# Optimization experiments

Hardware: AMD Instinct MI355X
Metric: run time of the kernel (lower is better)

## Reference

```python
import jax, jax.numpy as jnp
import numpy as np

B, S, H = 32, 4096, 768   # tuples, seq len, longformer hidden
N = 2048                  # total signals across all tuples (segments)
T = 16384                 # total pooled token indices (flattened ragged lists)
C = 32                    # char_size side features
D1, D2 = 512, 512         # MLP hidden dims


def setup_inputs() -> dict:
    key = jax.random.key(0)
    ks = jax.random.split(key, 9)
    hidden_states = jax.random.normal(ks[0], (B, S, H), dtype=jnp.float32)
    base_characteristics = jax.random.normal(ks[1], (N, C), dtype=jnp.float32)
    # MLP params: Linear(768+C,512) -> ReLU -> Linear(512,512) -> ReLU -> Linear(512,1) -> Sigmoid
    w1 = jax.random.normal(ks[2], (H + C, D1), dtype=jnp.float32) * 0.02
    b1 = jnp.zeros((D1,), dtype=jnp.float32)
    w2 = jax.random.normal(ks[3], (D1, D2), dtype=jnp.float32) * 0.02
    b2 = jnp.zeros((D2,), dtype=jnp.float32)
    w3 = jax.random.normal(ks[4], (D2, 1), dtype=jnp.float32) * 0.02
    b3 = jnp.zeros((1,), dtype=jnp.float32)
    # Flattened ragged pooling indices: token_indices index into flattened [B*S] tokens,
    # segment_ids map each index to its (tuple, signal) segment in [0, N).
    token_indices = jax.random.randint(ks[5], (T,), 0, B * S, dtype=jnp.int64)
    segment_ids = jnp.sort(jax.random.randint(ks[6], (T,), 0, N, dtype=jnp.int64))
    return {
        "hidden_states": hidden_states,
        "base_characteristics": base_characteristics,
        "w1": w1, "b1": b1, "w2": w2, "b2": b2, "w3": w3, "b3": b3,
        "token_indices": token_indices,
        "segment_ids": segment_ids,
    }


def reference(hidden_states, base_characteristics, w1, b1, w2, b2, w3, b3,
              token_indices, segment_ids):
    # Gather pooled token embeddings and segment-mean per signal.
    flat = hidden_states.reshape(-1, H)                       # [B*S, H]
    gathered = flat[token_indices]                            # [T, H]
    sums = jax.ops.segment_sum(gathered, segment_ids, num_segments=N)  # [N, H]
    counts = jax.ops.segment_sum(jnp.ones((T,), flat.dtype), segment_ids,
                                 num_segments=N)              # [N]
    pooled = sums / jnp.maximum(counts, 1.0)[:, None]         # mean pool per signal
    feats = jnp.concatenate([pooled, base_characteristics], axis=1)  # [N, H+C]
    h = jax.nn.relu(feats @ w1 + b1)
    h = jax.nn.relu(h @ w2 + b2)
    score = jax.nn.sigmoid(h @ w3 + b3)                       # [N, 1]
    return score.T                                            # [1, N], matches .T in torch
```

## Files before the change

kernel.cpp:

```cpp
#include <hip/hip_runtime.h>
#include <hip/hip_bf16.h>
#include <math.h>

#define BATCH 32
#define SEQ   4096
#define HID   768
#define CHR   32
#define NSEG  2048
#define TTOK  16384
#define KF    (HID + CHR)
#define D1    512
#define D2    512

__global__ __launch_bounds__(256) void pool_kernel(
    const float* __restrict__ hs,
    const float* __restrict__ basec,
    const int*   __restrict__ tok,
    const int*   __restrict__ seg,
    float*       __restrict__ feats)
{
    const int n   = blockIdx.x;
    const int tid = threadIdx.x;

    int lo;
    {
        int l = 0, r = TTOK;
        while (l < r) { int m = (l + r) >> 1; if (seg[m] < n) l = m + 1; else r = m; }
        lo = l;
    }
    int hi;
    {
        int l = lo, r = TTOK;
        while (l < r) { int m = (l + r) >> 1; if (seg[m] < n + 1) l = m + 1; else r = m; }
        hi = l;
    }

    float a0 = 0.f, a1 = 0.f, a2 = 0.f;
    for (int t = lo; t < hi; ++t) {
        const float* row = hs + (long)tok[t] * HID;
        a0 += row[tid];
        a1 += row[tid + 256];
        a2 += row[tid + 512];
    }
    const float inv = 1.0f / (float)((hi - lo) > 0 ? (hi - lo) : 1);
    float* frow = feats + (long)n * KF;
    frow[tid]       = a0 * inv;
    frow[tid + 256] = a1 * inv;
    frow[tid + 512] = a2 * inv;
    if (tid < CHR) frow[HID + tid] = basec[n * CHR + tid];
}

template <int BK>
__global__ __launch_bounds__(256) void gemm_bias_relu(
    const float* __restrict__ A,
    const float* __restrict__ B,
    const float* __restrict__ bias,
    float*       __restrict__ Cc,
    int M, int N, int K)
{
    __shared__ float As[BK][68];
    __shared__ float Bs[BK][68];

    const int tid = threadIdx.x;
    const int bm  = blockIdx.x * 64;
    const int bn  = blockIdx.y * 64;
    const int tx  = tid & 15;
    const int ty  = tid >> 4;

    float acc[4][4];
    #pragma unroll
    for (int i = 0; i < 4; ++i)
        #pragma unroll
        for (int j = 0; j < 4; ++j) acc[i][j] = 0.f;

    for (int k0 = 0; k0 < K; k0 += BK) {
        #pragma unroll
        for (int i = 0; i < (64 * BK) / 256; ++i) {
            int idx = tid + i * 256;
            int r = idx / BK, kk = idx % BK;
            As[kk][r] = A[(long)(bm + r) * K + (k0 + kk)];
        }
        #pragma unroll
        for (int i = 0; i < (64 * BK) / 256; ++i) {
            int idx = tid + i * 256;
            int kk = idx / 64, c = idx % 64;
            Bs[kk][c] = B[(long)(k0 + kk) * N + (bn + c)];
        }
        __syncthreads();

        #pragma unroll
        for (int kk = 0; kk < BK; ++kk) {
            float a[4], b[4];
            #pragma unroll
            for (int i = 0; i < 4; ++i) a[i] = As[kk][ty * 4 + i];
            #pragma unroll
            for (int j = 0; j < 4; ++j) b[j] = Bs[kk][tx * 4 + j];
            #pragma unroll
            for (int i = 0; i < 4; ++i)
                #pragma unroll
                for (int j = 0; j < 4; ++j)
                    acc[i][j] = fmaf(a[i], b[j], acc[i][j]);
        }
        __syncthreads();
    }

    #pragma unroll
    for (int i = 0; i < 4; ++i) {
        int row = bm + ty * 4 + i;
        #pragma unroll
        for (int j = 0; j < 4; ++j) {
            int col = bn + tx * 4 + j;
            float v = acc[i][j] + bias[col];
            Cc[(long)row * N + col] = fmaxf(v, 0.0f);
        }
    }
}

__global__ __launch_bounds__(256) void final_kernel(
    const float* __restrict__ h2,
    const float* __restrict__ w3,
    const float* __restrict__ b3,
    float*       __restrict__ out)
{
    const int wave = threadIdx.x >> 6;
    const int lane = threadIdx.x & 63;
    const int n = blockIdx.x * 4 + wave;
    if (n >= NSEG) return;

    const float* row = h2 + (long)n * D2;
    float s = 0.f;
    #pragma unroll
    for (int i = 0; i < D2 / 64; ++i)
        s = fmaf(row[lane + i * 64], w3[lane + i * 64], s);

    #pragma unroll
    for (int off = 32; off > 0; off >>= 1)
        s += __shfl_xor(s, off, 64);

    if (lane == 0) {
        float x = s + b3[0];
        out[n] = 1.0f / (1.0f + expf(-x));
    }
}

extern "C" void kernel_launch(void* const* d_in, const int* in_sizes, int n_in,
                              void* d_out, int out_size, void* d_ws, size_t ws_size,
                              hipStream_t stream) {
    const float* hs    = (const float*)d_in[0];
    const float* basec = (const float*)d_in[1];
    const float* w1    = (const float*)d_in[2];
    const float* b1    = (const float*)d_in[3];
    const float* w2    = (const float*)d_in[4];
    const float* b2    = (const float*)d_in[5];
    const float* w3    = (const float*)d_in[6];
    const float* b3    = (const float*)d_in[7];
    const int*   tok   = (const int*)d_in[8];
    const int*   seg   = (const int*)d_in[9];
    float*       out   = (float*)d_out;

    float* feats = (float*)d_ws;
    float* h1    = feats + (size_t)NSEG * KF;
    float* h2    = h1    + (size_t)NSEG * D1;

    pool_kernel<<<NSEG, 256, 0, stream>>>(hs, basec, tok, seg, feats);

    dim3 g1(NSEG / 64, D1 / 64);
    gemm_bias_relu<16><<<g1, 256, 0, stream>>>(feats, w1, b1, h1, NSEG, D1, KF);

    dim3 g2(NSEG / 64, D2 / 64);
    gemm_bias_relu<16><<<g2, 256, 0, stream>>>(h1, w2, b2, h2, NSEG, D2, D1);

    final_kernel<<<NSEG / 4, 256, 0, stream>>>(h2, w3, b3, out);
}
```

Before: 564.4 us.

## Run MLP GEMMs on bf16 MFMA with transposed bf16 weights

Pooled features and the first hidden layer are now stored in bf16, and the weights are transposed and converted to bf16 by a new kernel each call. The scalar FP32 tiled GEMM is replaced by an MFMA 16x16x32 bf16 kernel that uses swizzled shared memory and register prefetch of the next K tile. The aim is to cut GEMM compute time and halve intermediate memory traffic, at the cost of lower precision and two extra transpose launches.

New measurement: 490.1 us. -13.2%, faster.

```diff
diff --git a/kernel.cpp b/kernel.cpp
--- a/kernel.cpp
+++ b/kernel.cpp
@@ -2,22 +2,24 @@
 #include <hip/hip_bf16.h>
 #include <math.h>
 
-#define BATCH 32
-#define SEQ   4096
 #define HID   768
 #define CHR   32
 #define NSEG  2048
 #define TTOK  16384
-#define KF    (HID + CHR)
+#define KF    800
 #define D1    512
 #define D2    512
+
+typedef __hip_bfloat16 bf16;
+typedef __attribute__((ext_vector_type(8))) short short8;
+typedef __attribute__((ext_vector_type(4))) float floatx4;
 
 __global__ __launch_bounds__(256) void pool_kernel(
     const float* __restrict__ hs,
     const float* __restrict__ basec,
     const int*   __restrict__ tok,
     const int*   __restrict__ seg,
-    float*       __restrict__ feats)
+    bf16*        __restrict__ feats)
 {
     const int n   = blockIdx.x;
     const int tid = threadIdx.x;
@@ -43,75 +45,121 @@
         a2 += row[tid + 512];
     }
     const float inv = 1.0f / (float)((hi - lo) > 0 ? (hi - lo) : 1);
-    float* frow = feats + (long)n * KF;
-    frow[tid]       = a0 * inv;
-    frow[tid + 256] = a1 * inv;
-    frow[tid + 512] = a2 * inv;
-    if (tid < CHR) frow[HID + tid] = basec[n * CHR + tid];
-}
-
-template <int BK>
-__global__ __launch_bounds__(256) void gemm_bias_relu(
-    const float* __restrict__ A,
-    const float* __restrict__ B,
+    bf16* frow = feats + (long)n * KF;
+    frow[tid]       = __float2bfloat16(a0 * inv);
+    frow[tid + 256] = __float2bfloat16(a1 * inv);
+    frow[tid + 512] = __float2bfloat16(a2 * inv);
+    if (tid < CHR) frow[HID + tid] = __float2bfloat16(basec[n * CHR + tid]);
+}
+
+__global__ __launch_bounds__(256) void transpose_convert(
+    const float* __restrict__ in,
+    bf16*        __restrict__ out,
+    int K, int N)
+{
+    __shared__ float tile[32][33];
+    const int k0 = blockIdx.x * 32;
+    const int n0 = blockIdx.y * 32;
+    const int tx = threadIdx.x & 31;
+    const int ty = threadIdx.x >> 5;
+
+    #pragma unroll
+    for (int i = 0; i < 32; i += 8)
+        tile[ty + i][tx] = in[(long)(k0 + ty + i) * N + (n0 + tx)];
+    __syncthreads();
+    #pragma unroll
+    for (int i = 0; i < 32; i += 8)
+        out[(long)(n0 + ty + i) * K + (k0 + tx)] = __float2bfloat16(tile[tx][ty + i]);
+}
+
+template <bool OUT_BF16>
+__global__ __launch_bounds__(256) void gemm_bt(
+    const bf16*  __restrict__ A,
+    const bf16*  __restrict__ Bt,
     const float* __restrict__ bias,
-    float*       __restrict__ Cc,
+    void*        __restrict__ Cout,
     int M, int N, int K)
 {
-    __shared__ float As[BK][68];
-    __shared__ float Bs[BK][68];
-
-    const int tid = threadIdx.x;
-    const int bm  = blockIdx.x * 64;
-    const int bn  = blockIdx.y * 64;
-    const int tx  = tid & 15;
-    const int ty  = tid >> 4;
-
-    float acc[4][4];
-    #pragma unroll
-    for (int i = 0; i < 4; ++i)
-        #pragma unroll
-        for (int j = 0; j < 4; ++j) acc[i][j] = 0.f;
-
-    for (int k0 = 0; k0 < K; k0 += BK) {
-        #pragma unroll
-        for (int i = 0; i < (64 * BK) / 256; ++i) {
-            int idx = tid + i * 256;
-            int r = idx / BK, kk = idx % BK;
-            As[kk][r] = A[(long)(bm + r) * K + (k0 + kk)];
-        }
-        #pragma unroll
-        for (int i = 0; i < (64 * BK) / 256; ++i) {
-            int idx = tid + i * 256;
-            int kk = idx / 64, c = idx % 64;
-            Bs[kk][c] = B[(long)(k0 + kk) * N + (bn + c)];
-        }
+    __shared__ short As[64 * 32];
+    __shared__ short Bs[64 * 32];
+
+    const int tid  = threadIdx.x;
+    const int bm   = blockIdx.x * 64;
+    const int bn   = blockIdx.y * 64;
+    const int wave = tid >> 6;
+    const int lane = tid & 63;
+    const int wm   = wave >> 1;
+    const int wn   = wave & 1;
+    const int g    = lane >> 4;
+    const int r    = lane & 15;
+
+    const int srow = tid >> 2;
+    const int sch  = tid & 3;
+    const int sidx = srow * 32 + ((sch * 8) ^ ((srow & 3) << 3));
+
+    const int nk = K / 32;
+
+    floatx4 acc[2][2];
+    #pragma unroll
+    for (int i = 0; i < 2; ++i)
+        #pragma unroll
+        for (int j = 0; j < 2; ++j) acc[i][j] = (floatx4){0.f, 0.f, 0.f, 0.f};
+
+    short8 areg = *(const short8*)(A  + (long)(bm + srow) * K + sch * 8);
+    short8 breg = *(const short8*)(Bt + (long)(bn + srow) * K + sch * 8);
+    *(short8*)(&As[sidx]) = areg;
+    *(short8*)(&Bs[sidx]) = breg;
+
+    for (int ks = 0; ks < nk; ++ks) {
         __syncthreads();
 
-        #pragma unroll
-        for (int kk = 0; kk < BK; ++kk) {
-            float a[4], b[4];
+        if (ks + 1 < nk) {
+            areg = *(const short8*)(A  + (long)(bm + srow) * K + (ks + 1) * 32 + sch * 8);
+            breg = *(const short8*)(Bt + (long)(bn + srow) * K + (ks + 1) * 32 + sch * 8);
+        }
+
+        short8 af[2], bf[2];
+        #pragma unroll
+        for (int fm = 0; fm < 2; ++fm) {
+            const int ar = wm * 32 + fm * 16 + r;
+            af[fm] = *(const short8*)(&As[ar * 32 + ((g * 8) ^ ((ar & 3) << 3))]);
+        }
+        #pragma unroll
+        for (int fn = 0; fn < 2; ++fn) {
+            const int br = wn * 32 + fn * 16 + r;
+            bf[fn] = *(const short8*)(&Bs[br * 32 + ((g * 8) ^ ((br & 3) << 3))]);
+        }
+        #pragma unroll
+        for (int fm = 0; fm < 2; ++fm)
             #pragma unroll
-            for (int i = 0; i < 4; ++i) a[i] = As[kk][ty * 4 + i];
+            for (int fn = 0; fn < 2; ++fn)
+                acc[fm][fn] = __builtin_amdgcn_mfma_f32_16x16x32_bf16(
+                    af[fm], bf[fn], acc[fm][fn], 0, 0, 0);
+
+        __syncthreads();
+
+        if (ks + 1 < nk) {
+            *(short8*)(&As[sidx]) = areg;
+            *(short8*)(&Bs[sidx]) = breg;
+        }
+    }
+
+    #pragma unroll
+    for (int fm = 0; fm < 2; ++fm) {
+        #pragma unroll
+        for (int fn = 0; fn < 2; ++fn) {
+            const int col = bn + wn * 32 + fn * 16 + r;
+            const float bv = bias[col];
             #pragma unroll
-            for (int j = 0; j < 4; ++j) b[j] = Bs[kk][tx * 4 + j];
-            #pragma unroll
-            for (int i = 0; i < 4; ++i)
-                #pragma unroll
-                for (int j = 0; j < 4; ++j)
-                    acc[i][j] = fmaf(a[i], b[j], acc[i][j]);
-        }
-        __syncthreads();
-    }
-
-    #pragma unroll
-    for (int i = 0; i < 4; ++i) {
-        int row = bm + ty * 4 + i;
-        #pragma unroll
-        for (int j = 0; j < 4; ++j) {
-            int col = bn + tx * 4 + j;
-            float v = acc[i][j] + bias[col];
-            Cc[(long)row * N + col] = fmaxf(v, 0.0f);
+            for (int j = 0; j < 4; ++j) {
+                const int row = bm + wm * 32 + fm * 16 + g * 4 + j;
+                float v = acc[fm][fn][j] + bv;
+                v = fmaxf(v, 0.0f);
+                if (OUT_BF16)
+                    ((bf16*)Cout)[(long)row * N + col] = __float2bfloat16(v);
+                else
+                    ((float*)Cout)[(long)row * N + col] = v;
+            }
         }
     }
 }
@@ -158,17 +206,22 @@
     const int*   seg   = (const int*)d_in[9];
     float*       out   = (float*)d_out;
 
-    float* feats = (float*)d_ws;
-    float* h1    = feats + (size_t)NSEG * KF;
-    float* h2    = h1    + (size_t)NSEG * D1;
+    char* ws = (char*)d_ws;
+    bf16* feats = (bf16*)ws;  ws += (size_t)NSEG * KF * 2;
+    bf16* w1t   = (bf16*)ws;  ws += (size_t)D1 * KF * 2;
+    bf16* w2t   = (bf16*)ws;  ws += (size_t)D2 * D1 * 2;
+    bf16* h1    = (bf16*)ws;  ws += (size_t)NSEG * D1 * 2;
+    float* h2   = (float*)ws;
 
     pool_kernel<<<NSEG, 256, 0, stream>>>(hs, basec, tok, seg, feats);
 
-    dim3 g1(NSEG / 64, D1 / 64);
-    gemm_bias_relu<16><<<g1, 256, 0, stream>>>(feats, w1, b1, h1, NSEG, D1, KF);
-
-    dim3 g2(NSEG / 64, D2 / 64);
-    gemm_bias_relu<16><<<g2, 256, 0, stream>>>(h1, w2, b2, h2, NSEG, D2, D1);
+    transpose_convert<<<dim3(KF / 32, D1 / 32), 256, 0, stream>>>(w1, w1t, KF, D1);
+    transpose_convert<<<dim3(D1 / 32, D2 / 32), 256, 0, stream>>>(w2, w2t, D1, D2);
+
+    gemm_bt<true ><<<dim3(NSEG / 64, D1 / 64), 256, 0, stream>>>(
+        feats, w1t, b1, (void*)h1, NSEG, D1, KF);
+    gemm_bt<false><<<dim3(NSEG / 64, D2 / 64), 256, 0, stream>>>(
+        h1, w2t, b2, (void*)h2, NSEG, D2, D1);
 
     final_kernel<<<NSEG / 4, 256, 0, stream>>>(h2, w3, b3, out);
 }
```
